# Kernel tuning notes

Hardware: AMD Instinct MI355X
Metric: run time of the kernel (lower is better)

Reference implementation:

```python
import jax, jax.numpy as jnp
import numpy as np

BATCH = 262144  # number of trajectories
# strictly increasing keyframe indices spanning frames 0..48 (n=13 knots, m=48 outputs)
KNOTS = np.array([0, 3, 7, 12, 16, 21, 25, 28, 32, 36, 41, 45, 48], dtype=np.int32)


def setup_inputs() -> dict:
    key = jax.random.key(0)
    index = jnp.asarray(KNOTS)
    value = jax.random.normal(key, (BATCH, KNOTS.shape[0], 2), dtype=jnp.float32)
    return {"index": index, "value": value}


def reference(index, value):
    # index is an integer knot vector -> treat as static (defines output length m).
    idx = np.asarray(index)
    m = int(idx[-1] - idx[0])
    # output sample points: start point excluded, end point included
    p = idx[0] + np.arange(1, m + 1)            # (m,)
    # segment i covers (idx[i], idx[i+1]]
    seg = np.searchsorted(idx, p, side="left") - 1  # (m,)

    pf = jnp.asarray(p, dtype=value.dtype)
    x0 = jnp.asarray(idx[seg], dtype=value.dtype)
    x1 = jnp.asarray(idx[seg + 1], dtype=value.dtype)
    t = ((pf - x0) / (x1 - x0))[:, None]        # (m, 1)

    start = value[..., seg, :]                  # (..., m, 2) gathered knot starts
    end = value[..., seg + 1, :]                # (..., m, 2) gathered knot ends
    return start + (end - start) * t
```

## Files before the change

### kernel.cpp

```cpp
#include <hip/hip_runtime.h>


__global__ __launch_bounds__(256)
void LinearInterpolation_20907900797406_kernel(
    const int* __restrict__ index,
    const float2* __restrict__ value,
    float4* __restrict__ out,
    int batch, int nk, int m) {
  __shared__ int   s_idx[32];
  __shared__ int   s_seg[64];
  __shared__ float s_t[64];

  const int tid = threadIdx.x;
  if (tid < nk) s_idx[tid] = index[tid];
  __syncthreads();
  if (tid < m) {
    const int p = s_idx[0] + tid + 1;
    int cnt = 0;
    #pragma unroll 13
    for (int k = 0; k < nk; ++k) cnt += (s_idx[k] < p) ? 1 : 0;
    const int seg = cnt - 1;
    s_seg[tid] = seg;
    s_t[tid] = (float)(p - s_idx[seg]) / (float)(s_idx[seg + 1] - s_idx[seg]);
  }
  __syncthreads();

  const int half = m >> 1;
  const long long gid = (long long)blockIdx.x * blockDim.x + tid;
  const long long total = (long long)batch * half;
  if (gid >= total) return;

  const int b  = (int)(gid / half);
  const int jp = (int)(gid - (long long)b * half);
  const int j0 = jp * 2;
  const int j1 = j0 + 1;

  const float2* vb = value + (long long)b * nk;
  const int s0 = s_seg[j0], s1 = s_seg[j1];
  const float t0 = s_t[j0], t1 = s_t[j1];

  const float2 a0 = vb[s0], e0 = vb[s0 + 1];
  const float2 a1 = vb[s1], e1 = vb[s1 + 1];

  float4 o;
  o.x = a0.x + (e0.x - a0.x) * t0;
  o.y = a0.y + (e0.y - a0.y) * t0;
  o.z = a1.x + (e1.x - a1.x) * t1;
  o.w = a1.y + (e1.y - a1.y) * t1;
  out[gid] = o;
}

extern "C" void kernel_launch(void* const* d_in, const int* in_sizes, int n_in,
                              void* d_out, int out_size, void* d_ws, size_t ws_size,
                              hipStream_t stream) {
  const int*   index = (const int*)d_in[0];
  const float* value = (const float*)d_in[1];
  float*       out   = (float*)d_out;

  const int nk    = in_sizes[0];
  const int batch = in_sizes[1] / (nk * 2);
  const int m     = out_size / (batch * 2);
  const int half  = m / 2;

  const long long total = (long long)batch * half;
  const int block = 256;
  const int grid  = (int)((total + block - 1) / block);

  LinearInterpolation_20907900797406_kernel<<<grid, block, 0, stream>>>(
      index, (const float2*)value, (float4*)out, batch, nk, m);
}
```

Before: 140.2 us.

## Stage per-block batch values in LDS with coalesced float4 loads

Each block now handles 64 trajectories. It copies their knot values into shared memory with contiguous float4 loads, then computes interpolated pairs from LDS and writes output with coalesced stores. This replaces per-thread scattered float2 global gathers, which were duplicated across outputs. The cost is an extra barrier and LDS traffic per block, plus fewer, larger blocks.

Result: faster. 128.7 us (-8.2%).

```diff
diff --git a/kernel.cpp b/kernel.cpp
--- a/kernel.cpp
+++ b/kernel.cpp
@@ -1,15 +1,18 @@
 #include <hip/hip_runtime.h>
 
+
+#define BPB 64
 
 __global__ __launch_bounds__(256)
 void LinearInterpolation_20907900797406_kernel(
     const int* __restrict__ index,
-    const float2* __restrict__ value,
-    float4* __restrict__ out,
+    const float* __restrict__ value,
+    float4* __restrict__ out4,
     int batch, int nk, int m) {
   __shared__ int   s_idx[32];
   __shared__ int   s_seg[64];
   __shared__ float s_t[64];
+  __shared__ float s_val[BPB * 32];
 
   const int tid = threadIdx.x;
   if (tid < nk) s_idx[tid] = index[tid];
@@ -23,31 +26,41 @@
     s_seg[tid] = seg;
     s_t[tid] = (float)(p - s_idx[seg]) / (float)(s_idx[seg + 1] - s_idx[seg]);
   }
+
+  const int b0 = blockIdx.x * BPB;
+  const int nb = min(BPB, batch - b0);
+  const int nfl = nb * nk * 2;
+  const int nf4 = nfl >> 2;
+  const float4* src4 = (const float4*)(value + (long long)b0 * nk * 2);
+  float4* s_val4 = (float4*)s_val;
+  for (int i = tid; i < nf4; i += 256) s_val4[i] = src4[i];
+  if (tid < (nfl & 3)) {
+    s_val[(nf4 << 2) + tid] = value[(long long)b0 * nk * 2 + (nf4 << 2) + tid];
+  }
   __syncthreads();
 
   const int half = m >> 1;
-  const long long gid = (long long)blockIdx.x * blockDim.x + tid;
-  const long long total = (long long)batch * half;
-  if (gid >= total) return;
-
-  const int b  = (int)(gid / half);
-  const int jp = (int)(gid - (long long)b * half);
-  const int j0 = jp * 2;
-  const int j1 = j0 + 1;
-
-  const float2* vb = value + (long long)b * nk;
-  const int s0 = s_seg[j0], s1 = s_seg[j1];
-  const float t0 = s_t[j0], t1 = s_t[j1];
-
-  const float2 a0 = vb[s0], e0 = vb[s0 + 1];
-  const float2 a1 = vb[s1], e1 = vb[s1 + 1];
-
-  float4 o;
-  o.x = a0.x + (e0.x - a0.x) * t0;
-  o.y = a0.y + (e0.y - a0.y) * t0;
-  o.z = a1.x + (e1.x - a1.x) * t1;
-  o.w = a1.y + (e1.y - a1.y) * t1;
-  out[gid] = o;
+  const int npairs = nb * half;
+  const long long outBase = (long long)b0 * half;
+  const int row = nk * 2;
+  for (int off = tid; off < npairs; off += 256) {
+    const int bl = off / half;
+    const int jp = off - bl * half;
+    const float* vb = &s_val[bl * row];
+    const int j0 = jp * 2;
+    const int sa = s_seg[j0], sb = s_seg[j0 + 1];
+    const float ta = s_t[j0], tb = s_t[j0 + 1];
+    const float2 a0 = *(const float2*)&vb[2 * sa];
+    const float2 e0 = *(const float2*)&vb[2 * sa + 2];
+    const float2 a1 = *(const float2*)&vb[2 * sb];
+    const float2 e1 = *(const float2*)&vb[2 * sb + 2];
+    float4 o;
+    o.x = a0.x + (e0.x - a0.x) * ta;
+    o.y = a0.y + (e0.y - a0.y) * ta;
+    o.z = a1.x + (e1.x - a1.x) * tb;
+    o.w = a1.y + (e1.y - a1.y) * tb;
+    out4[outBase + off] = o;
+  }
 }
 
 extern "C" void kernel_launch(void* const* d_in, const int* in_sizes, int n_in,
@@ -60,12 +73,8 @@
   const int nk    = in_sizes[0];
   const int batch = in_sizes[1] / (nk * 2);
   const int m     = out_size / (batch * 2);
-  const int half  = m / 2;
 
-  const long long total = (long long)batch * half;
-  const int block = 256;
-  const int grid  = (int)((total + block - 1) / block);
-
-  LinearInterpolation_20907900797406_kernel<<<grid, block, 0, stream>>>(
-      index, (const float2*)value, (float4*)out, batch, nk, m);
+  const int grid = (batch + BPB - 1) / BPB;
+  LinearInterpolation_20907900797406_kernel<<<grid, 256, 0, stream>>>(
+      index, value, (float4*)out, batch, nk, m);
 }
```
